# Kernel tuning notes

Hardware: AMD Instinct MI355X
Metric: run time of the kernel (lower is better)

The kernel has to match this reference:

```python
import jax, jax.numpy as jnp
import numpy as np

A = -0.75  # torch bicubic cubic-convolution coefficient

def _cubic_k(t):
    at = jnp.abs(t)
    return jnp.where(at <= 1, (A + 2) * at**3 - (A + 3) * at**2 + 1,
           jnp.where(at < 2, A * at**3 - 5 * A * at**2 + 8 * A * at - 4 * A, 0.0))

def _resize_last(x, out_size):
    # bicubic, align_corners=True, along last axis
    in_size = x.shape[-1]
    pos = jnp.arange(out_size, dtype=x.dtype) * ((in_size - 1) / (out_size - 1))
    i0 = jnp.floor(pos).astype(jnp.int32)
    frac = pos - i0
    offs = jnp.arange(-1, 3, dtype=jnp.int32)                    # 4 taps
    idx = jnp.clip(i0[None] + offs[:, None], 0, in_size - 1)     # [4, out]
    w = _cubic_k(frac[None] - offs[:, None].astype(x.dtype))     # [4, out]
    g = x[..., idx]                                              # [..., 4, out]
    return jnp.einsum('...ko,ko->...o', g, w)

def bicubic(x, H, W):
    x = _resize_last(x, W)
    x = jnp.swapaxes(_resize_last(jnp.swapaxes(x, -1, -2), H), -1, -2)
    return x

def conv(x, w, b):
    y = jax.lax.conv_general_dilated(x, w, (1, 1), 'SAME',
                                     dimension_numbers=('NCHW', 'OIHW', 'NCHW'))
    return y + b[None, :, None, None]

def pool(x):
    return jax.lax.reduce_window(x, -jnp.inf, jax.lax.max, (1, 1, 2, 2), (1, 1, 2, 2), 'VALID')

def extract(x, ws, bs):
    # feat1: vgg19 features[:2]
    x1 = jax.nn.relu(conv(x, ws[0], bs[0]))
    # feat2: vgg19 features[2:18]
    h = jax.nn.relu(conv(x1, ws[1], bs[1])); h = pool(h)
    h = jax.nn.relu(conv(h, ws[2], bs[2]))
    h = jax.nn.relu(conv(h, ws[3], bs[3])); h = pool(h)
    for i in range(4, 8):
        h = jax.nn.relu(conv(h, ws[i], bs[i]))
    h = bicubic(h, x1.shape[-2], x1.shape[-1])
    return jnp.concatenate([x1, h], axis=1)  # [B, 320, H, W]

def normalizer(f1, f2):
    B, C = f1.shape[:2]
    a = f1.reshape(B, C, -1)
    b = f2.reshape(B, C, -1)
    xc = jnp.concatenate([a, b], axis=-1)
    mean = xc.mean(-1, keepdims=True)
    std = xc.mean(-1, keepdims=True)  # faithful to original source bug: std = mean
    a = (a - mean) / (std + 1e-8)
    b = (b - mean) / (std + 1e-8)
    return a.reshape(f1.shape), b.reshape(f2.shape)

_CHANS = [(3, 64), (64, 64), (64, 128), (128, 128), (128, 256), (256, 256), (256, 256), (256, 256)]

def setup_inputs() -> dict:
    key = jax.random.key(0)
    ks = jax.random.split(key, 20)
    inp = {}
    for i, (ci, co) in enumerate(_CHANS):
        inp[f'w{i}'] = jax.random.normal(ks[i], (co, ci, 3, 3), jnp.float32) * np.sqrt(2.0 / (ci * 9))
        inp[f'b{i}'] = jnp.zeros((co,), jnp.float32)
    inp['x_ref'] = jax.random.normal(ks[16], (2, 3, 96, 96), jnp.float32)
    inp['x_template'] = jax.random.normal(ks[17], (2, 3, 48, 48), jnp.float32)
    inp['coef_ref'] = jnp.float32(1.0)
    inp['coef_tmp'] = jnp.float32(1.0)
    return inp

def reference(x_ref, x_template, coef_ref, coef_tmp,
              w0, b0, w1, b1, w2, b2, w3, b3, w4, b4, w5, b5, w6, b6, w7, b7):
    ws = [w0, w1, w2, w3, w4, w5, w6, w7]
    bs = [b0, b1, b2, b3, b4, b5, b6, b7]
    fref = extract(x_ref, ws, bs)
    ftem = extract(x_template, ws, bs)
    fref, ftem = normalizer(fref, ftem)
    B, C, m, n = fref.shape
    _, _, p, q = ftem.shape
    dist = jnp.einsum('bcmn,bcpq->bmnpq', fref, ftem).reshape(B, m * n, p * q)
    conf_ref = jax.nn.softmax(coef_ref * dist, axis=-2)
    conf_tmp = jax.nn.softmax(coef_tmp * dist, axis=-1)
    confidence = jnp.sqrt(conf_ref * conf_tmp)
    vals, _ = jax.lax.top_k(confidence, 10)
    values = vals.mean(-1, keepdims=True).reshape(B, m, n, 1)
    return values
```

## Files before the change

kernel.cpp:

```cpp
#include <hip/hip_runtime.h>
#include <math.h>

#define CK_A (-0.75f)

typedef __attribute__((ext_vector_type(8))) short bf16x8;
typedef __attribute__((ext_vector_type(4))) float f32x4;

struct CImg { const float* in; float* out; int H, W, tiles; long inBS, outBS, sStride; };

__device__ __forceinline__ float cubicw(float t){
  float at = fabsf(t);
  float at2 = at*at, at3 = at2*at;
  if (at <= 1.f) return (CK_A+2.f)*at3 - (CK_A+3.f)*at2 + 1.f;
  if (at < 2.f)  return CK_A*at3 - 5.f*CK_A*at2 + 8.f*CK_A*at - 4.f*CK_A;
  return 0.f;
}

__device__ __forceinline__ unsigned short f2bf_rne(float f){
  unsigned int u = __float_as_uint(f);
  unsigned int r = (u + 0x7fffu + ((u>>16)&1u)) >> 16;
  return (unsigned short)r;
}
__device__ __forceinline__ float bf2f(unsigned short h){
  return __uint_as_float(((unsigned int)h)<<16);
}

__device__ __forceinline__ void merge_ms(float& m, float& s, float m2, float s2){
  float M = fmaxf(m, m2);
  s = s*__expf(m - M) + s2*__expf(m2 - M);
  m = M;
}

#define MFB(a,b,c) __builtin_amdgcn_mfma_f32_16x16x32_bf16(a,b,c,0,0,0)

__global__ __launch_bounds__(256) void conv0_d(CImg A, CImg B,
    const float* __restrict__ w, const float* __restrict__ bias){
  bool isA = (int)blockIdx.x < A.tiles;
  const float* in = isA ? A.in : B.in;
  float* out = isA ? A.out : B.out;
  int H = isA ? A.H : B.H, W = isA ? A.W : B.W;
  long inBS = isA ? A.inBS : B.inBS, outBS = isA ? A.outBS : B.outBS;
  int tile = isA ? blockIdx.x : blockIdx.x - A.tiles;
  int tilesX = (W + 15) >> 4;
  int tx0 = (tile % tilesX) << 4, ty0 = (tile / tilesX) << 4;
  int cob = blockIdx.y * 4;
  int b = blockIdx.z;
  int lx = threadIdx.x & 15, ly = threadIdx.x >> 4;
  __shared__ float tile_s[3][18][20];
  float acc[4] = {0.f,0.f,0.f,0.f};
  const float* inb = in + (long)b*inBS;
  int ox = tx0+lx, oy = ty0+ly;

  for (int idx = threadIdx.x; idx < 3*324; idx += 256){
    int cl = idx/324, rem = idx - cl*324;
    int r = rem/18, c = rem - r*18;
    int gy = ty0 + r - 1, gx = tx0 + c - 1;
    const float* ic = inb + (long)cl*H*W;
    tile_s[cl][r][c] = (gy>=0 && gy<H && gx>=0 && gx<W) ? ic[(long)gy*W+gx] : 0.f;
  }
  __syncthreads();
  #pragma unroll
  for (int cl=0; cl<3; cl++){
    float t00=tile_s[cl][ly+0][lx+0], t01=tile_s[cl][ly+0][lx+1], t02=tile_s[cl][ly+0][lx+2];
    float t10=tile_s[cl][ly+1][lx+0], t11=tile_s[cl][ly+1][lx+1], t12=tile_s[cl][ly+1][lx+2];
    float t20=tile_s[cl][ly+2][lx+0], t21=tile_s[cl][ly+2][lx+1], t22=tile_s[cl][ly+2][lx+2];
    #pragma unroll
    for (int j=0;j<4;j++){
      const float* wp = w + ((long)(cob+j)*3 + cl)*9;
      float a = acc[j];
      a = fmaf(t00, wp[0], a); a = fmaf(t01, wp[1], a); a = fmaf(t02, wp[2], a);
      a = fmaf(t10, wp[3], a); a = fmaf(t11, wp[4], a); a = fmaf(t12, wp[5], a);
      a = fmaf(t20, wp[6], a); a = fmaf(t21, wp[7], a); a = fmaf(t22, wp[8], a);
      acc[j] = a;
    }
  }
  if (ox < W && oy < H){
    #pragma unroll
    for (int j=0;j<4;j++){
      float v = fmaxf(acc[j] + bias[cob+j], 0.f);
      out[(long)b*outBS + (long)(cob+j)*H*W + (long)oy*W + ox] = v;
    }
  }
}

__global__ void prep_w_all(const float* __restrict__ w1, const float* __restrict__ w2,
                           const float* __restrict__ w3, const float* __restrict__ w4,
                           const float* __restrict__ w5, const float* __restrict__ w6,
                           const float* __restrict__ w7, unsigned short* __restrict__ wp){
  const int ciT[7] = {64,64,128,128,256,256,256};
  const int coT[7] = {64,128,128,256,256,256,256};
  int l = blockIdx.y;
  const float* w = l==0?w1: l==1?w2: l==2?w3: l==3?w4: l==4?w5: l==5?w6: w7;
  long offv = 0;
  for (int i=0;i<7;i++){ if (i<l) offv += 9L*ciT[i]*coT[i]*2; }
  long total = 9L*ciT[l]*coT[l]*2;
  long e = (long)blockIdx.x*256 + threadIdx.x;
  if (e >= total) return;
  int CI = ciT[l], CO = coT[l];
  int j = (int)(e & 7);
  int lane = (int)((e>>3) & 63);
  int h = (int)((e>>9) & 1);
  long rem = e >> 10;
  int G = CO >> 4, KC = CI >> 5;
  int g = (int)(rem % G); long q = rem / G;
  int kc = (int)(q % KC); int o = (int)(q / KC);
  int co = (g<<4) + (lane & 15);
  int ci = (kc<<5) + ((lane>>4)<<3) + j;
  float v = w[((long)co*CI + ci)*9 + o];
  unsigned short hi = f2bf_rne(v);
  wp[offv + e] = (h==0) ? hi : f2bf_rne(v - bf2f(hi));
}

union AB { bf16x8 v; uint4 u; };

__global__ __launch_bounds__(256) void conv_mfma_d(
    CImg A, CImg B, const unsigned short* __restrict__ Wp,
    const float* __restrict__ bias, int CI, int CO, int nci, int S)
{
  bool isA = (int)blockIdx.x < A.tiles;
  const float* in = isA ? A.in : B.in;
  float* out = isA ? A.out : B.out;
  int H = isA ? A.H : B.H, W = isA ? A.W : B.W;
  long inBS = isA ? A.inBS : B.inBS, outBS = isA ? A.outBS : B.outBS;
  long sStride = isA ? A.sStride : B.sStride;
  int tile = isA ? blockIdx.x : blockIdx.x - A.tiles;

  int HW = H*W;
  int tilesX = (W+7)>>3;
  int tx0 = (tile % tilesX)<<3, ty0 = (tile / tilesX)<<3;
  int cobase = blockIdx.y << 6;
  int s = blockIdx.z % S, b = blockIdx.z / S;
  int tid = threadIdx.x, lane = tid & 63, wid = tid>>6;
  int wm = wid>>1, wn = wid&1;
  int KC = CI>>5, G = CO>>4;
  __shared__ __align__(16) unsigned short Bth[4000];
  __shared__ __align__(16) unsigned short Btl[4000];
  const float* inb = in + (long)b*inBS;

  int sofs[13]; int sla[13];
  #pragma unroll
  for (int i=0;i<13;i++){
    int e = tid + i*256;
    int cidx = e / 100, pix = e - cidx*100;
    int hy = pix/10, hx = pix - hy*10;
    int gy = ty0 - 1 + hy, gx = tx0 - 1 + hx;
    bool v = (gy>=0) && (gy<H) && (gx>=0) && (gx<W);
    sofs[i] = v ? (cidx*HW + gy*W + gx) : -1;
    sla[i] = pix*40 + cidx;
  }

  int n15 = lane & 15;
  int klane8 = (lane>>4)<<3;
  int p0 = wn*32 + n15;
  int base0 = ((p0>>3)*10 + (p0&7))*40 + klane8;
  int p1 = p0 + 16;
  int base1 = ((p1>>3)*10 + (p1&7))*40 + klane8;
  int g0 = (cobase>>4) + wm*2;

  f32x4 acc[2][2];
  #pragma unroll
  for (int i=0;i<2;i++)
    #pragma unroll
    for (int j=0;j<2;j++) acc[i][j] = (f32x4){0.f,0.f,0.f,0.f};

  int nkc = nci >> 5;
  for (int kk=0; kk<nkc; kk++){
    int ci0 = s*nci + (kk<<5);
    __syncthreads();
    #pragma unroll
    for (int i=0;i<12;i++){
      float v = (sofs[i] >= 0) ? inb[(long)ci0*HW + sofs[i]] : 0.f;
      unsigned short h = f2bf_rne(v);
      Bth[sla[i]] = h;
      Btl[sla[i]] = f2bf_rne(v - bf2f(h));
    }
    if (tid < 128){
      float v = (sofs[12] >= 0) ? inb[(long)ci0*HW + sofs[12]] : 0.f;
      unsigned short h = f2bf_rne(v);
      Bth[sla[12]] = h;
      Btl[sla[12]] = f2bf_rne(v - bf2f(h));
    }
    __syncthreads();
    int kc = ci0 >> 5;
    const unsigned short* wpb = Wp + (long)kc*G*1024 + (long)lane*8;
    #pragma unroll
    for (int o=0;o<9;o++){
      const int dy = o/3, dx = o - dy*3;
      const int sh = (dy*10+dx)*40;
      const unsigned short* wo = wpb + (long)o*KC*G*1024;
      AB a0h,a0l,a1h,a1l, b0h,b0l,b1h,b1l;
      a0h.u = *(const uint4*)(wo + (long)g0*1024);
      a0l.u = *(const uint4*)(wo + (long)g0*1024 + 512);
      a1h.u = *(const uint4*)(wo + (long)(g0+1)*1024);
      a1l.u = *(const uint4*)(wo + (long)(g0+1)*1024 + 512);
      b0h.v = *(const bf16x8*)&Bth[base0 + sh];
      b0l.v = *(const bf16x8*)&Btl[base0 + sh];
      b1h.v = *(const bf16x8*)&Bth[base1 + sh];
      b1l.v = *(const bf16x8*)&Btl[base1 + sh];
      acc[0][0] = MFB(a0h.v, b0l.v, acc[0][0]);
      acc[0][0] = MFB(a0l.v, b0h.v, acc[0][0]);
      acc[0][0] = MFB(a0h.v, b0h.v, acc[0][0]);
      acc[0][1] = MFB(a0h.v, b1l.v, acc[0][1]);
      acc[0][1] = MFB(a0l.v, b1h.v, acc[0][1]);
      acc[0][1] = MFB(a0h.v, b1h.v, acc[0][1]);
      acc[1][0] = MFB(a1h.v, b0l.v, acc[1][0]);
      acc[1][0] = MFB(a1l.v, b0h.v, acc[1][0]);
      acc[1][0] = MFB(a1h.v, b0h.v, acc[1][0]);
      acc[1][1] = MFB(a1h.v, b1l.v, acc[1][1]);
      acc[1][1] = MFB(a1l.v, b1h.v, acc[1][1]);
      acc[1][1] = MFB(a1h.v, b1h.v, acc[1][1]);
    }
  }

  float* outp = out + (long)s*sStride + (long)b*outBS;
  #pragma unroll
  for (int ng=0; ng<2; ng++){
    int p = wn*32 + ng*16 + n15;
    int gy = ty0 + (p>>3), gx = tx0 + (p&7);
    bool ok = (gy<H) && (gx<W);
    #pragma unroll
    for (int mg=0; mg<2; mg++){
      #pragma unroll
      for (int r=0;r<4;r++){
        if (ok){
          int co = cobase + wm*32 + mg*16 + ((lane>>4)<<2) + r;
          float v = acc[mg][ng][r];
          if (bias) v = fmaxf(v + bias[co], 0.f);
          outp[(long)co*HW + (long)gy*W + gx] = v;
        }
      }
    }
  }
}

__global__ void reduce_d(const float* __restrict__ pA, const float* __restrict__ pB,
                         const float* __restrict__ bias,
                         float* __restrict__ oA, float* __restrict__ oB,
                         int S, long sStrA, long sStrB, int CO, int HWa, int HWb,
                         long oBSa, long oBSb){
  int img = blockIdx.y;
  const float* part = img ? pB : pA;
  float* out = img ? oB : oA;
  int HW = img ? HWb : HWa;
  long sStride = img ? sStrB : sStrA;
  long outBS = img ? oBSb : oBSa;
  long tot = 2L*CO*HW;
  long e = (long)blockIdx.x*256 + threadIdx.x;
  if (e >= tot) return;
  long b = e / ((long)CO*HW);
  long r = e - b*(long)CO*HW;
  float v = 0.f;
  for (int s=0;s<S;s++) v += part[(long)s*sStride + e];
  int co = (int)(r / HW);
  out[b*outBS + r] = fmaxf(v + bias[co], 0.f);
}

__global__ void maxpool2_d(const float* __restrict__ inA, float* __restrict__ outA, long NCa, int HiA, int WiA,
                           const float* __restrict__ inB, float* __restrict__ outB, long NCb, int HiB, int WiB){
  const float* in = blockIdx.y ? inB : inA;
  float* out = blockIdx.y ? outB : outA;
  long NC = blockIdx.y ? NCb : NCa;
  int Hi = blockIdx.y ? HiB : HiA, Wi = blockIdx.y ? WiB : WiA;
  int Ho = Hi>>1, Wo = Wi>>1;
  long total = NC * Ho * Wo;
  long idx = (long)blockIdx.x*256 + threadIdx.x;
  if (idx >= total) return;
  int x = (int)(idx % Wo); long t = idx / Wo; int y = (int)(t % Ho); long nc = t / Ho;
  const float* p = in + (nc*Hi + 2*y)*(long)Wi + 2*x;
  out[idx] = fmaxf(fmaxf(p[0], p[1]), fmaxf(p[Wi], p[Wi+1]));
}

__global__ __launch_bounds__(256) void bicubic_d(
    const float* __restrict__ inA, float* __restrict__ outA,
    const float* __restrict__ inB, float* __restrict__ outB){
  int c = blockIdx.x;
  int img = blockIdx.y >> 1, b = blockIdx.y & 1;
  const float* in = img ? inB : inA;
  float* out = img ? outB : outA;
  int Hin = img ? 12 : 24, Win = Hin, Hout = img ? 48 : 96, Wout = Hout;
  long inBS = img ? 256L*144 : 256L*576;
  long outBS = img ? 320L*2304 : 320L*9216;
  __shared__ float s[576];
  const float* ip = in + (long)b*inBS + (long)c*Hin*Win;
  float* op = out + (long)b*outBS + (long)c*Hout*Wout;
  int n = Hin*Win;
  for (int i = threadIdx.x; i < n; i += 256) s[i] = ip[i];
  __syncthreads();
  float scy = (float)((double)(Hin-1)/(double)(Hout-1));
  float scx = scy;
  int total = Hout*Wout;
  for (int idx = threadIdx.x; idx < total; idx += 256){
    int ox = idx % Wout, oy = idx / Wout;
    float py = oy * scy, px = ox * scx;
    float iy0f = floorf(py), ix0f = floorf(px);
    int iy0 = (int)iy0f, ix0 = (int)ix0f;
    float fy = py - iy0f, fx = px - ix0f;
    float wy[4], wx[4]; int xs[4], ys[4];
    #pragma unroll
    for (int t=0;t<4;t++){
      wy[t] = cubicw(fy - (float)(t-1));
      wx[t] = cubicw(fx - (float)(t-1));
      ys[t] = min(max(iy0 + t - 1, 0), Hin-1);
      xs[t] = min(max(ix0 + t - 1, 0), Win-1);
    }
    float acc = 0.f;
    #pragma unroll
    for (int i=0;i<4;i++){
      const float* row = &s[ys[i]*Win];
      float rs = wx[0]*row[xs[0]] + wx[1]*row[xs[1]] + wx[2]*row[xs[2]] + wx[3]*row[xs[3]];
      acc = fmaf(wy[i], rs, acc);
    }
    op[idx] = acc;
  }
}

__global__ __launch_bounds__(256) void mean_k(const float* __restrict__ fR, const float* __restrict__ fT, float* __restrict__ mean){
  int c = blockIdx.x % 320, b = blockIdx.x / 320;
  const float* a = fR + ((long)b*320+c)*9216L;
  const float* t = fT + ((long)b*320+c)*2304L;
  float s = 0.f;
  for (int i=threadIdx.x;i<9216;i+=256) s += a[i];
  for (int i=threadIdx.x;i<2304;i+=256) s += t[i];
  __shared__ float sm[4];
  for (int o=32;o;o>>=1) s += __shfl_down(s,o);
  int lane = threadIdx.x & 63, wv = threadIdx.x >> 6;
  if (lane==0) sm[wv] = s;
  __syncthreads();
  if (threadIdx.x==0) mean[b*320+c] = (sm[0]+sm[1]+sm[2]+sm[3]) * (1.f/11520.f);
}

__global__ __launch_bounds__(256) void split_bf16_d(const float* __restrict__ fR, const float* __restrict__ fT,
    const float* __restrict__ mean,
    unsigned short* __restrict__ AhR, unsigned short* __restrict__ AlR,
    unsigned short* __restrict__ BhT, unsigned short* __restrict__ BlT){
  bool isR = blockIdx.x < 288;
  const float* feat = isR ? fR : fT;
  unsigned short* oh = isR ? AhR : BhT;
  unsigned short* ol = isR ? AlR : BlT;
  int P = isR ? 9216 : 2304;
  int m0 = (isR ? blockIdx.x : blockIdx.x - 288) * 32;
  int b = blockIdx.y;
  __shared__ unsigned int t[32][321];
  int ml = threadIdx.x & 31, kq = threadIdx.x >> 5;
  const float* fp = feat + (long)b*320*P + m0 + ml;
  for (int k = kq*40; k < kq*40+40; k++){
    float mu = mean[b*320+k];
    float v = (fp[(long)k*P] - mu) / (mu + 1e-8f);
    unsigned short h = f2bf_rne(v);
    unsigned short l = f2bf_rne(v - bf2f(h));
    t[ml][k] = ((unsigned int)h<<16) | l;
  }
  __syncthreads();
  long base = ((long)b*P + m0)*320;
  for (int idx = threadIdx.x; idx < 32*320; idx += 256){
    int m = idx/320, k = idx - m*320;
    unsigned int p = t[m][k];
    oh[base + (long)m*320 + k] = (unsigned short)(p>>16);
    ol[base + (long)m*320 + k] = (unsigned short)(p & 0xffffu);
  }
}

union FragU { bf16x8 v; uint2 u[2]; };

__global__ __launch_bounds__(256) void gemm_mfma(
    const unsigned short* __restrict__ Ah, const unsigned short* __restrict__ Al,
    const unsigned short* __restrict__ Bh, const unsigned short* __restrict__ Bl,
    float* __restrict__ D, const float* __restrict__ coefr,
    float* __restrict__ pm, float* __restrict__ ps){
  const int N = 2304, K = 320;
  int n0 = blockIdx.x*128, m0 = blockIdx.y*128;
  __shared__ unsigned short As[2][128][36], Bs[2][128][36];
  int tid = threadIdx.x, lane = tid & 63, wid = tid >> 6;
  int wm = wid >> 1, wn = wid & 1;
  f32x4 acc[4][4];
  #pragma unroll
  for (int i=0;i<4;i++)
    #pragma unroll
    for (int j=0;j<4;j++) acc[i][j] = (f32x4){0.f,0.f,0.f,0.f};

  for (int k0=0; k0<K; k0+=32){
    #pragma unroll
    for (int q=0;q<2;q++){
      int flat = q*256 + tid;
      int row = flat >> 2, seg = flat & 3;
      long ga = (long)(m0+row)*K + k0 + seg*8;
      long gb = (long)(n0+row)*K + k0 + seg*8;
      uint4 va = *(const uint4*)(Ah + ga);
      *(uint2*)&As[0][row][seg*8]   = make_uint2(va.x, va.y);
      *(uint2*)&As[0][row][seg*8+4] = make_uint2(va.z, va.w);
      uint4 vb = *(const uint4*)(Al + ga);
      *(uint2*)&As[1][row][seg*8]   = make_uint2(vb.x, vb.y);
      *(uint2*)&As[1][row][seg*8+4] = make_uint2(vb.z, vb.w);
      uint4 vc = *(const uint4*)(Bh + gb);
      *(uint2*)&Bs[0][row][seg*8]   = make_uint2(vc.x, vc.y);
      *(uint2*)&Bs[0][row][seg*8+4] = make_uint2(vc.z, vc.w);
      uint4 vd = *(const uint4*)(Bl + gb);
      *(uint2*)&Bs[1][row][seg*8]   = make_uint2(vd.x, vd.y);
      *(uint2*)&Bs[1][row][seg*8+4] = make_uint2(vd.z, vd.w);
    }
    __syncthreads();

    FragU af[2][4], bf[2][4];
    #pragma unroll
    for (int g=0; g<4; g++){
      const unsigned short* pa0 = &As[0][wm*64 + g*16 + (lane&15)][(lane>>4)*4];
      const unsigned short* pa1 = &As[1][wm*64 + g*16 + (lane&15)][(lane>>4)*4];
      const unsigned short* pb0 = &Bs[0][wn*64 + g*16 + (lane&15)][(lane>>4)*4];
      const unsigned short* pb1 = &Bs[1][wn*64 + g*16 + (lane&15)][(lane>>4)*4];
      af[0][g].u[0] = *(const uint2*)pa0; af[0][g].u[1] = *(const uint2*)(pa0 + 16);
      af[1][g].u[0] = *(const uint2*)pa1; af[1][g].u[1] = *(const uint2*)(pa1 + 16);
      bf[0][g].u[0] = *(const uint2*)pb0; bf[0][g].u[1] = *(const uint2*)(pb0 + 16);
      bf[1][g].u[0] = *(const uint2*)pb1; bf[1][g].u[1] = *(const uint2*)(pb1 + 16);
    }
    #pragma unroll
    for (int mg=0; mg<4; mg++)
      #pragma unroll
      for (int ng=0; ng<4; ng++){
        acc[mg][ng] = MFB(af[0][mg].v, bf[1][ng].v, acc[mg][ng]);
        acc[mg][ng] = MFB(af[1][mg].v, bf[0][ng].v, acc[mg][ng]);
        acc[mg][ng] = MFB(af[0][mg].v, bf[0][ng].v, acc[mg][ng]);
      }
    __syncthreads();
  }

  #pragma unroll
  for (int mg=0; mg<4; mg++)
    #pragma unroll
    for (int ng=0; ng<4; ng++){
      int col = n0 + wn*64 + ng*16 + (lane & 15);
      #pragma unroll
      for (int r=0;r<4;r++){
        int rowv = m0 + wm*64 + mg*16 + (lane>>4)*4 + r;
        D[(long)rowv*N + col] = acc[mg][ng][r];
      }
    }

  float cr = *coefr;
  float* red = (float*)&As[0][0][0];
  float pmv[4], psv[4];
  #pragma unroll
  for (int ng=0; ng<4; ng++){
    float m = -INFINITY;
    #pragma unroll
    for (int mg=0; mg<4; mg++)
      #pragma unroll
      for (int r=0;r<4;r++) m = fmaxf(m, cr*acc[mg][ng][r]);
    float s = 0.f;
    #pragma unroll
    for (int mg=0; mg<4; mg++)
      #pragma unroll
      for (int r=0;r<4;r++) s += __expf(cr*acc[mg][ng][r] - m);
    #pragma unroll
    for (int o=16;o<64;o<<=1){
      float m2 = __shfl_xor(m,o), s2 = __shfl_xor(s,o);
      merge_ms(m,s,m2,s2);
    }
    pmv[ng]=m; psv[ng]=s;
  }
  if ((lane>>4)==0){
    #pragma unroll
    for (int ng=0; ng<4; ng++){
      int cl = wn*64 + ng*16 + lane;
      red[wm*128 + cl] = pmv[ng];
      red[256 + wm*128 + cl] = psv[ng];
    }
  }
  __syncthreads();
  if (wm==0 && (lane>>4)==0){
    #pragma unroll
    for (int ng=0; ng<4; ng++){
      int cl = wn*64 + ng*16 + lane;
      float m = pmv[ng], s = psv[ng];
      merge_ms(m, s, red[128+cl], red[384+cl]);
      pm[(long)blockIdx.y*2304 + n0 + cl] = m;
      ps[(long)blockIdx.y*2304 + n0 + cl] = s;
    }
  }
}

__global__ void colstat_merge(const float* __restrict__ pm, const float* __restrict__ ps,
                              float* __restrict__ qcol){
  int idx = blockIdx.x*256 + threadIdx.x;
  if (idx >= 2304) return;
  float m=-INFINITY, s=0.f;
  for (int k=0;k<72;k++) merge_ms(m, s, pm[(long)k*2304+idx], ps[(long)k*2304+idx]);
  qcol[idx] = 0.5f*m + 0.5f*__logf(s);
}

__global__ __launch_bounds__(256) void conf_topk_f(const float* __restrict__ D,
    const float* __restrict__ coefr, const float* __restrict__ coeft,
    const float* __restrict__ qcol, float* __restrict__ outp){
  int m = blockIdx.x;
  const float* drow = D + (long)m*2304;
  int tid = threadIdx.x, lane = tid & 63, wv = tid >> 6;
  float ct = *coeft, cr = *coefr;
  float v[9], tv[9];
  #pragma unroll
  for (int i=0;i<9;i++){ v[i] = drow[tid + i*256]; tv[i] = ct * v[i]; }

  __shared__ float sred[8];
  __shared__ unsigned int cand[40];

  float mx = tv[0];
  #pragma unroll
  for (int i=1;i<9;i++) mx = fmaxf(mx, tv[i]);
  #pragma unroll
  for (int o=1;o<64;o<<=1) mx = fmaxf(mx, __shfl_xor(mx, o));
  if (lane==0) sred[wv] = mx;
  __syncthreads();
  mx = fmaxf(fmaxf(sred[0],sred[1]), fmaxf(sred[2],sred[3]));
  float s = 0.f;
  #pragma unroll
  for (int i=0;i<9;i++) s += __expf(tv[i]-mx);
  #pragma unroll
  for (int o=1;o<64;o<<=1) s += __shfl_xor(s, o);
  if (lane==0) sred[4+wv] = s;
  __syncthreads();
  float rs = sred[4]+sred[5]+sred[6]+sred[7];
  float rho = 0.5f*mx + 0.5f*__logf(rs);
  float hc = 0.5f*(cr+ct);

  unsigned int key[9];
  #pragma unroll
  for (int i=0;i<9;i++){
    int n = i*256 + tid;
    float t = fmaf(hc, v[i], -qcol[n]);
    unsigned int b = __float_as_uint(t);
    b ^= (b >> 31) ? 0xFFFFFFFFu : 0x80000000u;
    key[i] = (b & 0xFFFFF000u) | (unsigned)n;
  }

  for (int t10=0; t10<10; t10++){
    unsigned int lb = key[0];
    #pragma unroll
    for (int i=1;i<9;i++) lb = lb > key[i] ? lb : key[i];
    unsigned int wb = lb;
    #pragma unroll
    for (int o=1;o<64;o<<=1){
      unsigned int x = (unsigned int)__shfl_xor((int)wb, o);
      wb = wb > x ? wb : x;
    }
    if (lane==0) cand[wv*10 + t10] = wb;
    #pragma unroll
    for (int i=0;i<9;i++) if (key[i]==wb) key[i]=0;
  }
  __syncthreads();

  if (wv == 0){
    unsigned int k = (lane < 40) ? cand[lane] : 0u;
    int sel = -1;
    for (int t10=0; t10<10; t10++){
      unsigned int wb = k;
      #pragma unroll
      for (int o=1;o<64;o<<=1){
        unsigned int x = (unsigned int)__shfl_xor((int)wb, o);
        wb = wb > x ? wb : x;
      }
      if (k == wb) k = 0;
      if (lane == t10) sel = (int)(wb & 0xFFFu);
    }
    float c = 0.f;
    if (sel >= 0){
      float t = fmaf(hc, drow[sel], -qcol[sel]);
      c = __expf(t - rho);
    }
    #pragma unroll
    for (int o=1;o<64;o<<=1) c += __shfl_xor(c, o);
    if (lane == 0) outp[m] = c * 0.1f;
  }
}

extern "C" void kernel_launch(void* const* d_in, const int* in_sizes, int n_in,
                              void* d_out, int out_size, void* d_ws, size_t ws_size,
                              hipStream_t stream) {
  const float *W[8], *Bp[8], *xr, *xt, *cr, *ct;
  if (in_sizes[0] == 1728){
    for (int i=0;i<8;i++){ W[i]=(const float*)d_in[2*i]; Bp[i]=(const float*)d_in[2*i+1]; }
    xr=(const float*)d_in[16]; xt=(const float*)d_in[17];
    cr=(const float*)d_in[18]; ct=(const float*)d_in[19];
  } else {
    xr=(const float*)d_in[0]; xt=(const float*)d_in[1];
    cr=(const float*)d_in[2]; ct=(const float*)d_in[3];
    for (int i=0;i<8;i++){ W[i]=(const float*)d_in[4+2*i]; Bp[i]=(const float*)d_in[5+2*i]; }
  }

  const int convCI[8] = {3,64,64,128,128,256,256,256};
  const int convCO[8] = {64,64,128,128,256,256,256,256};
  long wpoff[8]; long wtot = 0;
  for (int l=1;l<8;l++){ wpoff[l] = wtot; wtot += 9L*convCI[l]*convCO[l]*2; }

  float* ws = (float*)d_ws;
  long off = 0;
  auto alloc = [&](long nfl){ float* p = ws + off; off += (nfl + 63) & ~63L; return p; };
  float* featR = alloc(2L*320*9216);
  float* featT = alloc(2L*320*2304);
  float* meanb = alloc(640);
  float* pm    = alloc(72L*2304);
  float* ps    = alloc(72L*2304);
  float* qcol  = alloc(2304);
  unsigned short* wp = (unsigned short*)alloc((wtot+1)/2);
  float* scratch = alloc(9216L*2304);
  if ((size_t)(off*4) > ws_size) return;

  unsigned short* AhR = (unsigned short*)alloc((2L*9216*320 + 1)/2);
  unsigned short* AlR = (unsigned short*)alloc((2L*9216*320 + 1)/2);
  unsigned short* BhT = (unsigned short*)alloc((2L*2304*320 + 1)/2);
  unsigned short* BlT = (unsigned short*)alloc((2L*2304*320 + 1)/2);
  if ((size_t)(off*4) > ws_size) return;

  float* rA = scratch;
  float* rB = rA + 1179648;
  float* rC = rB + 294912;
  float* rD = rC + 589824;
  float* rE = rD + 589824;
  float* rF = rE + 147456;
  float* rG = rF + 294912;
  float* a2 = rG + 294912;
  float* b2 = a2 + 294912;
  float* c2 = b2 + 73728;
  float* d2 = c2 + 147456;
  float* e2 = d2 + 147456;
  float* f2 = e2 + 36864;
  float* g2 = f2 + 73728;
  float* tPR = g2 + 73728;
  float* tPT = tPR + 1179648;
  float* dist = scratch;

  auto mkimg = [](const float* in, float* out, int H, int Wd, int tiles,
                  long inBS, long outBS, long sStr){
    CImg c; c.in=in; c.out=out; c.H=H; c.W=Wd; c.tiles=tiles;
    c.inBS=inBS; c.outBS=outBS; c.sStride=sStr; return c;
  };

  prep_w_all<<<dim3(4608,7), 256, 0, stream>>>(W[1],W[2],W[3],W[4],W[5],W[6],W[7], wp);

  {
    CImg A = mkimg(xr, featR, 96,96, 36, 3L*9216, 320L*9216, 0);
    CImg B = mkimg(xt, featT, 48,48, 9, 3L*2304, 320L*2304, 0);
    conv0_d<<<dim3(45,16,2), 256, 0, stream>>>(A, B, W[0], Bp[0]);
  }
  {
    CImg A = mkimg(featR, rA, 96,96, 144, 320L*9216, 64L*9216, 0);
    CImg B = mkimg(featT, a2, 48,48, 36, 320L*2304, 64L*2304, 0);
    conv_mfma_d<<<dim3(180,1,2), 256, 0, stream>>>(A,B, wp+wpoff[1], Bp[1], 64,64,64,1);
  }
  maxpool2_d<<<dim3(1152,2), 256, 0, stream>>>(rA,rB,128,96,96, a2,b2,128,48,48);
  {
    CImg A = mkimg(rB, tPR, 48,48, 36, 64L*2304, 128L*2304, 589824);
    CImg B = mkimg(b2, tPT, 24,24, 9, 64L*576, 128L*576, 147456);
    conv_mfma_d<<<dim3(45,2,4), 256, 0, stream>>>(A,B, wp+wpoff[2], nullptr, 64,128,32,2);
    reduce_d<<<dim3(2304,2), 256, 0, stream>>>(tPR,tPT,Bp[2], rC,c2, 2, 589824,147456, 128, 2304,576, 128L*2304, 128L*576);
  }
  {
    CImg A = mkimg(rC, tPR, 48,48, 36, 128L*2304, 128L*2304, 589824);
    CImg B = mkimg(c2, tPT, 24,24, 9, 128L*576, 128L*576, 147456);
    conv_mfma_d<<<dim3(45,2,4), 256, 0, stream>>>(A,B, wp+wpoff[3], nullptr, 128,128,64,2);
    reduce_d<<<dim3(2304,2), 256, 0, stream>>>(tPR,tPT,Bp[3], rD,d2, 2, 589824,147456, 128, 2304,576, 128L*2304, 128L*576);
  }
  maxpool2_d<<<dim3(576,2), 256, 0, stream>>>(rD,rE,256,48,48, d2,e2,256,24,24);
  {
    CImg A = mkimg(rE, tPR, 24,24, 9, 128L*576, 256L*576, 294912);
    CImg B = mkimg(e2, tPT, 12,12, 4, 128L*144, 256L*144, 73728);
    conv_mfma_d<<<dim3(13,4,8), 256, 0, stream>>>(A,B, wp+wpoff[4], nullptr, 128,256,32,4);
    reduce_d<<<dim3(1152,2), 256, 0, stream>>>(tPR,tPT,Bp[4], rF,f2, 4, 294912,73728, 256, 576,144, 256L*576, 256L*144);
  }
  const float* inR[3] = {rF, rG, rF};  float* outR[3] = {rG, rF, rG};
  const float* inT[3] = {f2, g2, f2};  float* outT[3] = {g2, f2, g2};
  for (int i=0;i<3;i++){
    int l = 5+i;
    CImg A = mkimg(inR[i], tPR, 24,24, 9, 256L*576, 256L*576, 294912);
    CImg B = mkimg(inT[i], tPT, 12,12, 4, 256L*144, 256L*144, 73728);
    conv_mfma_d<<<dim3(13,4,8), 256, 0, stream>>>(A,B, wp+wpoff[l], nullptr, 256,256,64,4);
    reduce_d<<<dim3(1152,2), 256, 0, stream>>>(tPR,tPT,Bp[l], outR[i],outT[i], 4, 294912,73728, 256, 576,144, 256L*576, 256L*144);
  }
  bicubic_d<<<dim3(256,4), 256, 0, stream>>>(rG, featR + 64L*9216, g2, featT + 64L*2304);

  mean_k<<<640, 256, 0, stream>>>(featR, featT, meanb);
  split_bf16_d<<<dim3(360,2), 256, 0, stream>>>(featR, featT, meanb, AhR, AlR, BhT, BlT);

  for (int b=0; b<2; b++){
    gemm_mfma<<<dim3(18,72), 256, 0, stream>>>(
        AhR + (long)b*9216*320, AlR + (long)b*9216*320,
        BhT + (long)b*2304*320, BlT + (long)b*2304*320, dist, cr, pm, ps);
    colstat_merge<<<dim3(9), 256, 0, stream>>>(pm, ps, qcol);
    conf_topk_f<<<dim3(9216), 256, 0, stream>>>(dist, cr, ct, qcol, (float*)d_out + (long)b*9216);
  }
}
```

Baseline: 467.4 us.

## Load GEMM A fragments directly from global and widen K tile to 64

```diff
diff --git a/kernel.cpp b/kernel.cpp
--- a/kernel.cpp
+++ b/kernel.cpp
@@ -360,8 +360,6 @@
   }
 }
 
-union FragU { bf16x8 v; uint2 u[2]; };
-
 __global__ __launch_bounds__(256) void gemm_mfma(
     const unsigned short* __restrict__ Ah, const unsigned short* __restrict__ Al,
     const unsigned short* __restrict__ Bh, const unsigned short* __restrict__ Bl,
@@ -369,65 +367,67 @@
     float* __restrict__ pm, float* __restrict__ ps){
   const int N = 2304, K = 320;
   int n0 = blockIdx.x*128, m0 = blockIdx.y*128;
-  __shared__ unsigned short As[2][128][36], Bs[2][128][36];
+  __shared__ __align__(16) unsigned short Bs[2][128][72];
   int tid = threadIdx.x, lane = tid & 63, wid = tid >> 6;
   int wm = wid >> 1, wn = wid & 1;
+  int n15 = lane & 15, q8 = (lane>>4)<<3;
   f32x4 acc[4][4];
   #pragma unroll
   for (int i=0;i<4;i++)
     #pragma unroll
     for (int j=0;j<4;j++) acc[i][j] = (f32x4){0.f,0.f,0.f,0.f};
 
-  for (int k0=0; k0<K; k0+=32){
-    #pragma unroll
-    for (int q=0;q<2;q++){
-      int flat = q*256 + tid;
-      int row = flat >> 2, seg = flat & 3;
-      long ga = (long)(m0+row)*K + k0 + seg*8;
-      long gb = (long)(n0+row)*K + k0 + seg*8;
-      uint4 va = *(const uint4*)(Ah + ga);
-      *(uint2*)&As[0][row][seg*8]   = make_uint2(va.x, va.y);
-      *(uint2*)&As[0][row][seg*8+4] = make_uint2(va.z, va.w);
-      uint4 vb = *(const uint4*)(Al + ga);
-      *(uint2*)&As[1][row][seg*8]   = make_uint2(vb.x, vb.y);
-      *(uint2*)&As[1][row][seg*8+4] = make_uint2(vb.z, vb.w);
-      uint4 vc = *(const uint4*)(Bh + gb);
-      *(uint2*)&Bs[0][row][seg*8]   = make_uint2(vc.x, vc.y);
-      *(uint2*)&Bs[0][row][seg*8+4] = make_uint2(vc.z, vc.w);
-      uint4 vd = *(const uint4*)(Bl + gb);
-      *(uint2*)&Bs[1][row][seg*8]   = make_uint2(vd.x, vd.y);
-      *(uint2*)&Bs[1][row][seg*8+4] = make_uint2(vd.z, vd.w);
-    }
+  const unsigned short* aRowH[4];
+  const unsigned short* aRowL[4];
+  #pragma unroll
+  for (int g=0; g<4; g++){
+    long row = m0 + wm*64 + g*16 + n15;
+    aRowH[g] = Ah + row*K + q8;
+    aRowL[g] = Al + row*K + q8;
+  }
+
+  for (int k0=0; k0<K; k0+=64){
     __syncthreads();
-
-    FragU af[2][4], bf[2][4];
-    #pragma unroll
-    for (int g=0; g<4; g++){
-      const unsigned short* pa0 = &As[0][wm*64 + g*16 + (lane&15)][(lane>>4)*4];
-      const unsigned short* pa1 = &As[1][wm*64 + g*16 + (lane&15)][(lane>>4)*4];
-      const unsigned short* pb0 = &Bs[0][wn*64 + g*16 + (lane&15)][(lane>>4)*4];
-      const unsigned short* pb1 = &Bs[1][wn*64 + g*16 + (lane&15)][(lane>>4)*4];
-      af[0][g].u[0] = *(const uint2*)pa0; af[0][g].u[1] = *(const uint2*)(pa0 + 16);
-      af[1][g].u[0] = *(const uint2*)pa1; af[1][g].u[1] = *(const uint2*)(pa1 + 16);
-      bf[0][g].u[0] = *(const uint2*)pb0; bf[0][g].u[1] = *(const uint2*)(pb0 + 16);
-      bf[1][g].u[0] = *(const uint2*)pb1; bf[1][g].u[1] = *(const uint2*)(pb1 + 16);
-    }
-    #pragma unroll
-    for (int mg=0; mg<4; mg++)
+    #pragma unroll
+    for (int i=0;i<8;i++){
+      int e = i*256 + tid;
+      int tsr = e >> 10;
+      int rem = e & 1023;
+      int row = rem >> 3, seg = rem & 7;
+      const unsigned short* src = tsr ? Bl : Bh;
+      uint4 v = *(const uint4*)(src + (long)(n0+row)*K + k0 + seg*8);
+      *(uint4*)&Bs[tsr][row][seg*8] = v;
+    }
+    __syncthreads();
+
+    #pragma unroll
+    for (int kk=0; kk<2; kk++){
+      int ko = k0 + kk*32;
+      AB af[2][4], bf[2][4];
       #pragma unroll
-      for (int ng=0; ng<4; ng++){
-        acc[mg][ng] = MFB(af[0][mg].v, bf[1][ng].v, acc[mg][ng]);
-        acc[mg][ng] = MFB(af[1][mg].v, bf[0][ng].v, acc[mg][ng]);
-        acc[mg][ng] = MFB(af[0][mg].v, bf[0][ng].v, acc[mg][ng]);
+      for (int g=0; g<4; g++){
+        af[0][g].u = *(const uint4*)(aRowH[g] + ko);
+        af[1][g].u = *(const uint4*)(aRowL[g] + ko);
+        bf[0][g].v = *(const bf16x8*)&Bs[0][wn*64 + g*16 + n15][kk*32 + q8];
+        bf[1][g].v = *(const bf16x8*)&Bs[1][wn*64 + g*16 + n15][kk*32 + q8];
       }
-    __syncthreads();
-  }
+      #pragma unroll
+      for (int mg=0; mg<4; mg++)
+        #pragma unroll
+        for (int ng=0; ng<4; ng++){
+          acc[mg][ng] = MFB(af[0][mg].v, bf[1][ng].v, acc[mg][ng]);
+          acc[mg][ng] = MFB(af[1][mg].v, bf[0][ng].v, acc[mg][ng]);
+          acc[mg][ng] = MFB(af[0][mg].v, bf[0][ng].v, acc[mg][ng]);
+        }
+    }
+  }
+  __syncthreads();
 
   #pragma unroll
   for (int mg=0; mg<4; mg++)
     #pragma unroll
     for (int ng=0; ng<4; ng++){
-      int col = n0 + wn*64 + ng*16 + (lane & 15);
+      int col = n0 + wn*64 + ng*16 + n15;
       #pragma unroll
       for (int r=0;r<4;r++){
         int rowv = m0 + wm*64 + mg*16 + (lane>>4)*4 + r;
@@ -436,7 +436,7 @@
     }
 
   float cr = *coefr;
-  float* red = (float*)&As[0][0][0];
+  float* red = (float*)&Bs[0][0][0];
   float pmv[4], psv[4];
   #pragma unroll
   for (int ng=0; ng<4; ng++){
```

After: 505.1 us. 8.1% more time.
